# Kernel tuning notes

Measured on AMD Instinct MI355X. Metric: run time of the kernel, lower is better.

The kernel has to match this reference:

```python
import jax, jax.numpy as jnp
import numpy as np

N, D, K, H = 100000, 128, 16, 8
EPS = 1e-5


def setup_inputs() -> dict:
    key = jax.random.key(0)
    ks = jax.random.split(key, 8)
    s = 0.02
    return {
        "x": jax.random.normal(ks[0], (N, D), jnp.float32),
        "attention_samples": jax.random.randint(ks[1], (N, K), 0, N),
        "in_proj_w": jax.random.normal(ks[2], (3 * D, D), jnp.float32) * s,
        "in_proj_b": jnp.zeros((3 * D,), jnp.float32),
        "out_w": jax.random.normal(ks[3], (D, D), jnp.float32) * s,
        "out_b": jnp.zeros((D,), jnp.float32),
        "w1": jax.random.normal(ks[4], (4 * D, D), jnp.float32) * s,
        "b1": jnp.zeros((4 * D,), jnp.float32),
        "w2": jax.random.normal(ks[5], (D, 4 * D), jnp.float32) * s,
        "b2": jnp.zeros((D,), jnp.float32),
        "g1": jnp.ones((D,), jnp.float32),
        "be1": jnp.zeros((D,), jnp.float32),
        "g2": jnp.ones((D,), jnp.float32),
        "be2": jnp.zeros((D,), jnp.float32),
    }


def _layernorm(x, g, b):
    m = jnp.mean(x, axis=-1, keepdims=True)
    v = jnp.mean(jnp.square(x - m), axis=-1, keepdims=True)
    return (x - m) * jax.lax.rsqrt(v + EPS) * g + b


def reference(x, attention_samples, in_proj_w, in_proj_b, out_w, out_b,
              w1, b1, w2, b2, g1, be1, g2, be2):
    n, d = x.shape
    h = H
    hd = d // h
    wq, wk, wv = jnp.split(in_proj_w, 3, axis=0)
    bq, bk, bv = jnp.split(in_proj_b, 3, axis=0)
    # per-node query (q_len = 1)
    q = (x @ wq.T + bq).reshape(n, h, hd)            # [N,H,hd]
    samp = x[attention_samples]                       # [N,K,D] gathered neighbors
    k_ = (samp @ wk.T + bk).reshape(n, -1, h, hd)     # [N,K,H,hd]
    v_ = (samp @ wv.T + bv).reshape(n, -1, h, hd)
    scores = jnp.einsum('nhd,nkhd->nhk', q, k_) / jnp.sqrt(jnp.float32(hd))
    attn = jax.nn.softmax(scores, axis=-1)
    ctx = jnp.einsum('nhk,nkhd->nhd', attn, v_).reshape(n, d)
    attn_out = ctx @ out_w.T + out_b
    y = _layernorm(x + attn_out, g1, be1)
    ff = jax.nn.relu(y @ w1.T + b1) @ w2.T + b2
    return _layernorm(y + ff, g2, be2)
```

## Files before the change

kernel.cpp:

```cpp
#include <hip/hip_runtime.h>
#include <hip/hip_bf16.h>

typedef __attribute__((ext_vector_type(8))) short short8;
typedef __attribute__((ext_vector_type(4))) float f32x4;
typedef __attribute__((ext_vector_type(2))) float f32x2;

#define EPS 1e-5f

__device__ __forceinline__ unsigned short f2bf(float f) {
    union { float f; unsigned u; } v; v.f = f;
    unsigned u = v.u;
    u += 0x7FFFu + ((u >> 16) & 1u);
    return (unsigned short)(u >> 16);
}
__device__ __forceinline__ float bflo(unsigned u) {
    union { unsigned u; float f; } v; v.u = u << 16; return v.f;
}
__device__ __forceinline__ float bfhi(unsigned u) {
    union { unsigned u; float f; } v; v.u = u & 0xffff0000u; return v.f;
}
__device__ __forceinline__ float bf2f(ushort u) {
    union { unsigned u; float f; } v; v.u = ((unsigned)u) << 16; return v.f;
}
__device__ __forceinline__ unsigned char f2fp8(float v) {
    return (unsigned char)(__builtin_amdgcn_cvt_pk_fp8_f32(v, v, 0, false) & 0xff);
}
__device__ __forceinline__ int sig(int p) {
    return (((p >> 2) & 1) << 4) | (((p >> 3) & 3) << 2) | (p & 3);
}

__device__ __forceinline__ short8 load_frag_f32(const float* __restrict__ p) {
    f32x4 a = *(const f32x4*)p;
    f32x4 b = *(const f32x4*)(p + 4);
    short8 r;
    r[0] = (short)f2bf(a[0]); r[1] = (short)f2bf(a[1]);
    r[2] = (short)f2bf(a[2]); r[3] = (short)f2bf(a[3]);
    r[4] = (short)f2bf(b[0]); r[5] = (short)f2bf(b[1]);
    r[6] = (short)f2bf(b[2]); r[7] = (short)f2bf(b[3]);
    return r;
}

__device__ __forceinline__ float dot16_q_k8(const ushort* q, const unsigned char* kp) {
    uint4 kw = *(const uint4*)kp;
    const unsigned* qd = (const unsigned*)q;
    f32x2 a, b; float s = 0.f;
    a = __builtin_amdgcn_cvt_pk_f32_fp8(kw.x, false);
    b = __builtin_amdgcn_cvt_pk_f32_fp8(kw.x, true);
    s += a[0]*bflo(qd[0]) + a[1]*bfhi(qd[0]) + b[0]*bflo(qd[1]) + b[1]*bfhi(qd[1]);
    a = __builtin_amdgcn_cvt_pk_f32_fp8(kw.y, false);
    b = __builtin_amdgcn_cvt_pk_f32_fp8(kw.y, true);
    s += a[0]*bflo(qd[2]) + a[1]*bfhi(qd[2]) + b[0]*bflo(qd[3]) + b[1]*bfhi(qd[3]);
    a = __builtin_amdgcn_cvt_pk_f32_fp8(kw.z, false);
    b = __builtin_amdgcn_cvt_pk_f32_fp8(kw.z, true);
    s += a[0]*bflo(qd[4]) + a[1]*bfhi(qd[4]) + b[0]*bflo(qd[5]) + b[1]*bfhi(qd[5]);
    a = __builtin_amdgcn_cvt_pk_f32_fp8(kw.w, false);
    b = __builtin_amdgcn_cvt_pk_f32_fp8(kw.w, true);
    s += a[0]*bflo(qd[6]) + a[1]*bfhi(qd[6]) + b[0]*bflo(qd[7]) + b[1]*bfhi(qd[7]);
    return s;
}

__global__ __launch_bounds__(256) void k_prep(
        const float* __restrict__ ipw, const float* __restrict__ ow,
        const float* __restrict__ w1, const float* __restrict__ w2,
        ushort* __restrict__ wqb, ushort* __restrict__ wcat) {
    int i = blockIdx.x * 256 + threadIdx.x;
    if (i < 49152) wqb[i] = f2bf(ipw[i]);
    if (i < 147456) {
        float v;
        if (i < 8192) {
            int r = i >> 6, s = (i >> 3) & 7, e = i & 7;
            v = ow[r*128 + ((s ^ (r & 7)) << 3) + e];
        } else if (i < 16384) {
            int j = i - 8192;
            int r = j >> 6, s = (j >> 3) & 7, e = j & 7;
            v = ow[r*128 + 64 + ((s ^ (r & 7)) << 3) + e];
        } else {
            int j = i - 16384;
            int kb = j >> 13, o = j & 8191;
            if (o < 4096) {
                int r = (o >> 7) & 31, k16 = (o >> 3) & 15, e = o & 7;
                int cp = ((k16 ^ (r & 7)) << 3) + e;
                int cs = (cp & ~31) | sig(cp & 31);
                v = w1[(kb*32 + r)*128 + cs];
            } else {
                int oo = o - 4096;
                int ch = (oo >> 10) & 3, rw = (oo >> 3) & 127, e = oo & 7;
                v = w2[rw*512 + kb*32 + sig(ch*8 + e)];
            }
        }
        wcat[i] = f2bf(v);
    }
}

__global__ __launch_bounds__(256) void k_qkv(
        const float* __restrict__ x, const ushort* __restrict__ w,
        const float* __restrict__ bias, ushort* __restrict__ qt,
        unsigned char* __restrict__ kv8, ushort* __restrict__ xb, int N) {
    const int wave = threadIdx.x >> 6, lane = threadIdx.x & 63;
    const int l16 = lane & 15, l4 = lane >> 4;
    const int base = blockIdx.x * 64;

    short8 af[4][4];
    #pragma unroll
    for (int mt = 0; mt < 4; ++mt) {
        int row = base + mt*16 + l16;
        int rc = row < N ? row : N - 1;
        const float* p = x + (size_t)rc*128 + l4*8;
        #pragma unroll
        for (int kb = 0; kb < 4; ++kb) af[mt][kb] = load_frag_f32(p + kb*32);
    }
    #pragma unroll
    for (int mt = 0; mt < 4; ++mt) {
        int row = base + mt*16 + l16;
        if (row < N) {
            #pragma unroll
            for (int kb = 0; kb < 4; ++kb)
                *(short8*)(xb + (size_t)row*128 + kb*32 + l4*8) = af[mt][kb];
        }
    }
    #pragma unroll
    for (int i = 0; i < 6; ++i) {
        int col = (wave*6 + i)*16 + l16;
        const ushort* pw = w + (size_t)col*128 + l4*8;
        short8 bf[4];
        #pragma unroll
        for (int kb = 0; kb < 4; ++kb) bf[kb] = *(const short8*)(pw + kb*32);
        float bv = bias[col];
        #pragma unroll
        for (int mt = 0; mt < 4; ++mt) {
            f32x4 acc = {0.f, 0.f, 0.f, 0.f};
            #pragma unroll
            for (int kb = 0; kb < 4; ++kb)
                acc = __builtin_amdgcn_mfma_f32_16x16x32_bf16(af[mt][kb], bf[kb], acc, 0, 0, 0);
            #pragma unroll
            for (int r = 0; r < 4; ++r) {
                int row = base + mt*16 + l4*4 + r;
                if (row < N) {
                    float v = acc[r] + bv;
                    if (col < 128) qt[(size_t)row*128 + col] = f2bf(v);
                    else kv8[(size_t)row*256 + (col - 128)] = f2fp8(v);
                }
            }
        }
    }
}

__global__ __launch_bounds__(256) void k_attn(
        ushort* __restrict__ qt, const unsigned char* __restrict__ kv8,
        const int* __restrict__ samp, int N) {
    __shared__ float aw[4][8][17];
    __shared__ int   ai[4][16];
    const int wave = threadIdx.x >> 6, lane = threadIdx.x & 63;
    const int n = blockIdx.x * 4 + wave;
    if (n >= N) return;
    const int k  = lane & 15;
    const int hp = lane >> 4;
    const int h0 = hp, h1 = hp + 4;

    const int idx = samp[(size_t)n*16 + k];
    const ushort* qrow = qt + (size_t)n*128;
    const unsigned char* krow = kv8 + (size_t)idx*256;

    float s0 = dot16_q_k8(qrow + h0*16, krow + h0*16);
    float s1 = dot16_q_k8(qrow + h1*16, krow + h1*16);
    s0 *= 0.25f; s1 *= 0.25f;
    float m0 = s0, m1 = s1;
    #pragma unroll
    for (int off = 1; off < 16; off <<= 1) {
        m0 = fmaxf(m0, __shfl_xor(m0, off));
        m1 = fmaxf(m1, __shfl_xor(m1, off));
    }
    float e0 = __expf(s0 - m0), e1 = __expf(s1 - m1);
    float d0 = e0, d1 = e1;
    #pragma unroll
    for (int off = 1; off < 16; off <<= 1) {
        d0 += __shfl_xor(d0, off);
        d1 += __shfl_xor(d1, off);
    }
    aw[wave][h0][k] = e0 / d0;
    aw[wave][h1][k] = e1 / d1;
    if (hp == 0) ai[wave][k] = idx;

    const int c = lane & 15;
    const int g = lane >> 4;
    const int h = c >> 1;

    int rows[4];
    #pragma unroll
    for (int b = 0; b < 4; ++b) rows[b] = ai[wave][g + b*4];
    uint2 vv[4];
    #pragma unroll
    for (int b = 0; b < 4; ++b)
        vv[b] = *(const uint2*)(kv8 + (size_t)(unsigned)rows[b]*256 + 128 + c*8);
    float wk[4];
    #pragma unroll
    for (int b = 0; b < 4; ++b) wk[b] = aw[wave][h][g + b*4];

    float a8[8] = {0.f,0.f,0.f,0.f,0.f,0.f,0.f,0.f};
    #pragma unroll
    for (int b = 0; b < 4; ++b) {
        f32x2 p;
        p = __builtin_amdgcn_cvt_pk_f32_fp8(vv[b].x, false);
        a8[0] = fmaf(wk[b], p[0], a8[0]); a8[1] = fmaf(wk[b], p[1], a8[1]);
        p = __builtin_amdgcn_cvt_pk_f32_fp8(vv[b].x, true);
        a8[2] = fmaf(wk[b], p[0], a8[2]); a8[3] = fmaf(wk[b], p[1], a8[3]);
        p = __builtin_amdgcn_cvt_pk_f32_fp8(vv[b].y, false);
        a8[4] = fmaf(wk[b], p[0], a8[4]); a8[5] = fmaf(wk[b], p[1], a8[5]);
        p = __builtin_amdgcn_cvt_pk_f32_fp8(vv[b].y, true);
        a8[6] = fmaf(wk[b], p[0], a8[6]); a8[7] = fmaf(wk[b], p[1], a8[7]);
    }
    #pragma unroll
    for (int i = 0; i < 8; ++i) {
        a8[i] += __shfl_xor(a8[i], 16);
        a8[i] += __shfl_xor(a8[i], 32);
    }
    if (lane < 16) {
        uint4 pack;
        pack.x = (unsigned)f2bf(a8[0]) | ((unsigned)f2bf(a8[1]) << 16);
        pack.y = (unsigned)f2bf(a8[2]) | ((unsigned)f2bf(a8[3]) << 16);
        pack.z = (unsigned)f2bf(a8[4]) | ((unsigned)f2bf(a8[5]) << 16);
        pack.w = (unsigned)f2bf(a8[6]) | ((unsigned)f2bf(a8[7]) << 16);
        *(uint4*)(qt + (size_t)n*128 + c*8) = pack;
    }
}

__global__ __launch_bounds__(256) void k_tail(
        const ushort* __restrict__ ctx, const float* __restrict__ ob,
        const ushort* __restrict__ xb,
        const float* __restrict__ g1, const float* __restrict__ be1,
        const ushort* __restrict__ wcat, const float* __restrict__ b1,
        const float* __restrict__ b2,
        const float* __restrict__ g2, const float* __restrict__ be2,
        float* __restrict__ out, int N) {
    __shared__ __align__(16) char smem[32768];
    const int tid = threadIdx.x;
    const int lane = tid & 63;
    const int l16 = lane & 15, l4 = lane >> 4;
    const int base = blockIdx.x * 128 + (tid >> 6) * 32;
    int row[2], rc[2];
    row[0] = base + l16;       rc[0] = row[0] < N ? row[0] : N - 1;
    row[1] = base + 16 + l16;  rc[1] = row[1] < N ? row[1] : N - 1;

    uint4 nx0, nx1, nx2, nx3;
    const uint4* wc4 = (const uint4*)wcat;
#define STAGE_LOAD(cidx) { const uint4* s4 = wc4 + (cidx)*1024; \
    nx0 = s4[tid]; nx1 = s4[256 + tid]; nx2 = s4[512 + tid]; nx3 = s4[768 + tid]; }
#define STAGE_WRITE(cidx) { char* d = smem + (((cidx)&1) << 14); \
    *(uint4*)(d + tid*16) = nx0; *(uint4*)(d + (256 + tid)*16) = nx1; \
    *(uint4*)(d + (512 + tid)*16) = nx2; *(uint4*)(d + (768 + tid)*16) = nx3; }

    STAGE_LOAD(0); STAGE_WRITE(0); STAGE_LOAD(1);
    __syncthreads();

    f32x4 acc[2][8];
    #pragma unroll
    for (int mt = 0; mt < 2; ++mt)
        #pragma unroll
        for (int nt = 0; nt < 8; ++nt) acc[mt][nt] = (f32x4){0.f,0.f,0.f,0.f};

    #pragma unroll
    for (int ph = 0; ph < 2; ++ph) {
        STAGE_WRITE(ph + 1); STAGE_LOAD(ph + 2);
        short8 cfp[2][2];
        #pragma unroll
        for (int mt = 0; mt < 2; ++mt)
            #pragma unroll
            for (int j = 0; j < 2; ++j)
                cfp[mt][j] = *(const short8*)(ctx + (size_t)rc[mt]*128 + (ph*2 + j)*32 + l4*8);
        char* cur = smem + ((ph & 1) << 14);
        #pragma unroll
        for (int nt = 0; nt < 8; ++nt) {
            #pragma unroll
            for (int j = 0; j < 2; ++j) {
                int slot = (j*4 + l4) ^ (l16 & 7);
                short8 wf = *(const short8*)(cur + (nt*16 + l16)*128 + slot*16);
                acc[0][nt] = __builtin_amdgcn_mfma_f32_16x16x32_bf16(wf, cfp[0][j], acc[0][nt], 0, 0, 0);
                acc[1][nt] = __builtin_amdgcn_mfma_f32_16x16x32_bf16(wf, cfp[1][j], acc[1][nt], 0, 0, 0);
            }
        }
        __syncthreads();
    }

    float sum0 = 0.f, sq0 = 0.f, sum1 = 0.f, sq1 = 0.f;
    #pragma unroll
    for (int nt = 0; nt < 8; ++nt) {
        f32x4 obv = *(const f32x4*)(ob + nt*16 + l4*4);
        uint2 xr0 = *(const uint2*)(xb + (size_t)rc[0]*128 + nt*16 + l4*4);
        uint2 xr1 = *(const uint2*)(xb + (size_t)rc[1]*128 + nt*16 + l4*4);
        acc[0][nt][0] += obv[0] + bflo(xr0.x);
        acc[0][nt][1] += obv[1] + bfhi(xr0.x);
        acc[0][nt][2] += obv[2] + bflo(xr0.y);
        acc[0][nt][3] += obv[3] + bfhi(xr0.y);
        acc[1][nt][0] += obv[0] + bflo(xr1.x);
        acc[1][nt][1] += obv[1] + bfhi(xr1.x);
        acc[1][nt][2] += obv[2] + bflo(xr1.y);
        acc[1][nt][3] += obv[3] + bfhi(xr1.y);
        #pragma unroll
        for (int r = 0; r < 4; ++r) {
            sum0 += acc[0][nt][r]; sq0 += acc[0][nt][r]*acc[0][nt][r];
            sum1 += acc[1][nt][r]; sq1 += acc[1][nt][r]*acc[1][nt][r];
        }
    }
    sum0 += __shfl_xor(sum0, 16); sum0 += __shfl_xor(sum0, 32);
    sq0  += __shfl_xor(sq0, 16);  sq0  += __shfl_xor(sq0, 32);
    sum1 += __shfl_xor(sum1, 16); sum1 += __shfl_xor(sum1, 32);
    sq1  += __shfl_xor(sq1, 16);  sq1  += __shfl_xor(sq1, 32);
    float mean[2], rstd[2];
    mean[0] = sum0 * (1.f/128.f);
    rstd[0] = rsqrtf(sq0*(1.f/128.f) - mean[0]*mean[0] + EPS);
    mean[1] = sum1 * (1.f/128.f);
    rstd[1] = rsqrtf(sq1*(1.f/128.f) - mean[1]*mean[1] + EPS);

    short8 yfrag[2][4];
    #pragma unroll
    for (int nt = 0; nt < 8; ++nt) {
        f32x4 gv = *(const f32x4*)(g1 + nt*16 + l4*4);
        f32x4 bv = *(const f32x4*)(be1 + nt*16 + l4*4);
        #pragma unroll
        for (int mt = 0; mt < 2; ++mt)
            #pragma unroll
            for (int r = 0; r < 4; ++r) {
                float yn = (acc[mt][nt][r] - mean[mt]) * rstd[mt] * gv[r] + bv[r];
                yfrag[mt][nt >> 1][(nt & 1)*4 + r] = (short)f2bf(yn);
            }
    }

    f32x4 (&acc2)[2][8] = acc;
    #pragma unroll
    for (int mt = 0; mt < 2; ++mt)
        #pragma unroll
        for (int nt = 0; nt < 8; ++nt) acc2[mt][nt] = (f32x4){0.f,0.f,0.f,0.f};

    #pragma unroll 2
    for (int p = 2; p < 18; ++p) {
        if (p <= 16) { STAGE_WRITE(p + 1); }
        if (p <= 15) { STAGE_LOAD(p + 2); }
        const int kb = p - 2;
        char* cur = smem + ((p & 1) << 14);
        short8 wA[4], wB[4];
        #pragma unroll
        for (int c = 0; c < 4; ++c) {
            int slot = (c*4 + l4) ^ (l16 & 7);
            wA[c] = *(const short8*)(cur + l16*256 + slot*16);
            wB[c] = *(const short8*)(cur + 4096 + l16*256 + slot*16);
        }
        f32x4 hA[2] = {{0.f,0.f,0.f,0.f},{0.f,0.f,0.f,0.f}};
        f32x4 hB[2] = {{0.f,0.f,0.f,0.f},{0.f,0.f,0.f,0.f}};
        #pragma unroll
        for (int c = 0; c < 4; ++c)
            #pragma unroll
            for (int mt = 0; mt < 2; ++mt) {
                hA[mt] = __builtin_amdgcn_mfma_f32_16x16x32_bf16(wA[c], yfrag[mt][c], hA[mt], 0, 0, 0);
                hB[mt] = __builtin_amdgcn_mfma_f32_16x16x32_bf16(wB[c], yfrag[mt][c], hB[mt], 0, 0, 0);
            }
        f32x4 bA = *(const f32x4*)(b1 + kb*32 + l4*4);
        f32x4 bB = *(const f32x4*)(b1 + kb*32 + 16 + l4*4);
        short8 hf[2];
        #pragma unroll
        for (int mt = 0; mt < 2; ++mt)
            #pragma unroll
            for (int r = 0; r < 4; ++r) {
                float vA = hA[mt][r] + bA[r]; vA = vA > 0.f ? vA : 0.f;
                float vB = hB[mt][r] + bB[r]; vB = vB > 0.f ? vB : 0.f;
                hf[mt][r]     = (short)f2bf(vA);
                hf[mt][4 + r] = (short)f2bf(vB);
            }
        #pragma unroll
        for (int nt = 0; nt < 8; ++nt) {
            short8 w2f = *(const short8*)(cur + 8192 + l4*2048 + (nt*16 + l16)*16);
            acc2[0][nt] = __builtin_amdgcn_mfma_f32_16x16x32_bf16(w2f, hf[0], acc2[0][nt], 0, 0, 0);
            acc2[1][nt] = __builtin_amdgcn_mfma_f32_16x16x32_bf16(w2f, hf[1], acc2[1][nt], 0, 0, 0);
        }
        if (p < 17) __syncthreads();
    }

    #pragma unroll
    for (int mt = 0; mt < 2; ++mt) {
        float sum2 = 0.f, sq2 = 0.f;
        #pragma unroll
        for (int nt = 0; nt < 8; ++nt) {
            f32x4 b2v = *(const f32x4*)(b2 + nt*16 + l4*4);
            #pragma unroll
            for (int r = 0; r < 4; ++r) {
                float s = bf2f((ushort)yfrag[mt][nt >> 1][(nt & 1)*4 + r]) + acc2[mt][nt][r] + b2v[r];
                acc2[mt][nt][r] = s; sum2 += s; sq2 += s*s;
            }
        }
        sum2 += __shfl_xor(sum2, 16); sum2 += __shfl_xor(sum2, 32);
        sq2  += __shfl_xor(sq2, 16);  sq2  += __shfl_xor(sq2, 32);
        float mean2 = sum2 * (1.f/128.f);
        float rstd2 = rsqrtf(sq2*(1.f/128.f) - mean2*mean2 + EPS);
        if (row[mt] < N) {
            #pragma unroll
            for (int nt = 0; nt < 8; ++nt) {
                f32x4 gv = *(const f32x4*)(g2 + nt*16 + l4*4);
                f32x4 bv = *(const f32x4*)(be2 + nt*16 + l4*4);
                f32x4 o;
                #pragma unroll
                for (int r = 0; r < 4; ++r)
                    o[r] = (acc2[mt][nt][r] - mean2) * rstd2 * gv[r] + bv[r];
                *(f32x4*)(out + (size_t)row[mt]*128 + nt*16 + l4*4) = o;
            }
        }
    }
#undef STAGE_LOAD
#undef STAGE_WRITE
}

extern "C" void kernel_launch(void* const* d_in, const int* in_sizes, int n_in,
                              void* d_out, int out_size, void* d_ws, size_t ws_size,
                              hipStream_t stream) {
    (void)n_in; (void)out_size; (void)ws_size;
    const float* x   = (const float*)d_in[0];
    const int*   smp = (const int*)  d_in[1];
    const float* ipw = (const float*)d_in[2];
    const float* ipb = (const float*)d_in[3];
    const float* ow  = (const float*)d_in[4];
    const float* ob  = (const float*)d_in[5];
    const float* w1  = (const float*)d_in[6];
    const float* b1  = (const float*)d_in[7];
    const float* w2  = (const float*)d_in[8];
    const float* b2  = (const float*)d_in[9];
    const float* g1  = (const float*)d_in[10];
    const float* be1 = (const float*)d_in[11];
    const float* g2  = (const float*)d_in[12];
    const float* be2 = (const float*)d_in[13];
    const int N = in_sizes[0] / 128;

    ushort* qt   = (ushort*)d_ws;
    unsigned char* kv8 = (unsigned char*)(qt + (size_t)N*128);
    ushort* wqb  = (ushort*)(kv8 + (size_t)N*256);
    ushort* wcat = wqb + 384*128;
    ushort* xb   = wcat + 18*8192;
    float*  outp = (float*)d_out;

    k_prep <<<576,         256, 0, stream>>>(ipw, ow, w1, w2, wqb, wcat);
    k_qkv  <<<(N+63)/64,   256, 0, stream>>>(x, wqb, ipb, qt, kv8, xb, N);
    k_attn <<<(N+3)/4,     256, 0, stream>>>(qt, kv8, smp, N);
    k_tail <<<(N+127)/128, 256, 0, stream>>>(qt, ob, xb, g1, be1,
                                             wcat, b1, b2, g2, be2, outp, N);
}
```

Before: 236.5 us.

## Switch tail GEMMs to FP8 MFMA with resident weights and persistent blocks

Weights for out-proj, FFN1 and FFN2 are pre-scaled and stored as FP8, then loaded once into 144KB of LDS by a persistent 256-block, 512-thread tail kernel that loops over row tiles. The context vector is written as scaled FP8, and all tail matmuls use fp8 MFMA with rescaling afterwards. The qkv kernel also stages its outputs in shared memory so q and kv8 are written with coalesced vector stores. The aim is to halve weight and context traffic, remove per-stage weight streaming and barriers, and raise MFMA throughput, at the cost of FP8 accuracy loss in the activations and the FFN hidden layer.

```diff
diff --git a/kernel.cpp b/kernel.cpp
--- a/kernel.cpp
+++ b/kernel.cpp
@@ -24,6 +24,11 @@
 }
 __device__ __forceinline__ unsigned char f2fp8(float v) {
     return (unsigned char)(__builtin_amdgcn_cvt_pk_fp8_f32(v, v, 0, false) & 0xff);
+}
+__device__ __forceinline__ unsigned pk4fp8(float a, float b, float c, float d) {
+    unsigned u = __builtin_amdgcn_cvt_pk_fp8_f32(a, b, 0, false);
+    u = __builtin_amdgcn_cvt_pk_fp8_f32(c, d, u, true);
+    return u;
 }
 __device__ __forceinline__ int sig(int p) {
     return (((p >> 2) & 1) << 4) | (((p >> 3) & 3) << 2) | (p & 3);
@@ -62,33 +67,26 @@
 __global__ __launch_bounds__(256) void k_prep(
         const float* __restrict__ ipw, const float* __restrict__ ow,
         const float* __restrict__ w1, const float* __restrict__ w2,
-        ushort* __restrict__ wqb, ushort* __restrict__ wcat) {
+        ushort* __restrict__ wqb, unsigned char* __restrict__ wcat8) {
     int i = blockIdx.x * 256 + threadIdx.x;
     if (i < 49152) wqb[i] = f2bf(ipw[i]);
     if (i < 147456) {
         float v;
-        if (i < 8192) {
-            int r = i >> 6, s = (i >> 3) & 7, e = i & 7;
-            v = ow[r*128 + ((s ^ (r & 7)) << 3) + e];
-        } else if (i < 16384) {
-            int j = i - 8192;
-            int r = j >> 6, s = (j >> 3) & 7, e = j & 7;
-            v = ow[r*128 + 64 + ((s ^ (r & 7)) << 3) + e];
+        if (i < 16384) {
+            int r = i >> 7, s = (i >> 3) & 15, e = i & 7;
+            v = ow[r*128 + ((s ^ (r & 15)) << 3) + e];
+        } else if (i < 81920) {
+            int j = i - 16384;
+            int kb = j >> 12, r = (j >> 7) & 31, s = (j >> 3) & 15, e = j & 7;
+            int cp = ((s ^ (r & 15)) << 3) + e;
+            int cs = (cp & ~31) | sig(cp & 31);
+            v = w1[(kb*32 + r)*128 + cs];
         } else {
-            int j = i - 16384;
-            int kb = j >> 13, o = j & 8191;
-            if (o < 4096) {
-                int r = (o >> 7) & 31, k16 = (o >> 3) & 15, e = o & 7;
-                int cp = ((k16 ^ (r & 7)) << 3) + e;
-                int cs = (cp & ~31) | sig(cp & 31);
-                v = w1[(kb*32 + r)*128 + cs];
-            } else {
-                int oo = o - 4096;
-                int ch = (oo >> 10) & 3, rw = (oo >> 3) & 127, e = oo & 7;
-                v = w2[rw*512 + kb*32 + sig(ch*8 + e)];
-            }
-        }
-        wcat[i] = f2bf(v);
+            int j = i - 81920;
+            int kb = j >> 12, ch = (j >> 10) & 3, rw = (j >> 3) & 127, e = j & 7;
+            v = w2[rw*512 + kb*32 + sig(ch*8 + e)];
+        }
+        wcat8[i] = f2fp8(16.f * v);
     }
 }
 
@@ -96,6 +94,7 @@
         const float* __restrict__ x, const ushort* __restrict__ w,
         const float* __restrict__ bias, ushort* __restrict__ qt,
         unsigned char* __restrict__ kv8, ushort* __restrict__ xb, int N) {
+    __shared__ ushort sls[64 * 392];
     const int wave = threadIdx.x >> 6, lane = threadIdx.x & 63;
     const int l16 = lane & 15, l4 = lane >> 4;
     const int base = blockIdx.x * 64;
@@ -133,13 +132,31 @@
             for (int kb = 0; kb < 4; ++kb)
                 acc = __builtin_amdgcn_mfma_f32_16x16x32_bf16(af[mt][kb], bf[kb], acc, 0, 0, 0);
             #pragma unroll
-            for (int r = 0; r < 4; ++r) {
-                int row = base + mt*16 + l4*4 + r;
-                if (row < N) {
-                    float v = acc[r] + bv;
-                    if (col < 128) qt[(size_t)row*128 + col] = f2bf(v);
-                    else kv8[(size_t)row*256 + (col - 128)] = f2fp8(v);
-                }
+            for (int r = 0; r < 4; ++r)
+                sls[(mt*16 + l4*4 + r)*392 + col] = f2bf(acc[r] + bv);
+        }
+    }
+    __syncthreads();
+    {
+        const int row = threadIdx.x >> 2, q = threadIdx.x & 3;
+        const int grow = base + row;
+        if (grow < N) {
+            const ushort* sp = sls + row*392;
+            #pragma unroll
+            for (int j = 0; j < 4; ++j) {
+                uint4 v = *(const uint4*)(sp + q*32 + j*8);
+                *(uint4*)(qt + (size_t)grow*128 + q*32 + j*8) = v;
+            }
+            #pragma unroll
+            for (int j = 0; j < 4; ++j) {
+                unsigned wds[4];
+                #pragma unroll
+                for (int h = 0; h < 4; ++h) {
+                    const ushort* e = sp + 128 + q*64 + j*16 + h*4;
+                    wds[h] = pk4fp8(bf2f(e[0]), bf2f(e[1]), bf2f(e[2]), bf2f(e[3]));
+                }
+                *(uint4*)(kv8 + (size_t)grow*256 + q*64 + j*16) =
+                    make_uint4(wds[0], wds[1], wds[2], wds[3]);
             }
         }
     }
@@ -215,196 +232,201 @@
         a8[i] += __shfl_xor(a8[i], 32);
     }
     if (lane < 16) {
-        uint4 pack;
-        pack.x = (unsigned)f2bf(a8[0]) | ((unsigned)f2bf(a8[1]) << 16);
-        pack.y = (unsigned)f2bf(a8[2]) | ((unsigned)f2bf(a8[3]) << 16);
-        pack.z = (unsigned)f2bf(a8[4]) | ((unsigned)f2bf(a8[5]) << 16);
-        pack.w = (unsigned)f2bf(a8[6]) | ((unsigned)f2bf(a8[7]) << 16);
-        *(uint4*)(qt + (size_t)n*128 + c*8) = pack;
-    }
-}
-
-__global__ __launch_bounds__(256) void k_tail(
-        const ushort* __restrict__ ctx, const float* __restrict__ ob,
+        unsigned lo = pk4fp8(8.f*a8[0], 8.f*a8[1], 8.f*a8[2], 8.f*a8[3]);
+        unsigned hi = pk4fp8(8.f*a8[4], 8.f*a8[5], 8.f*a8[6], 8.f*a8[7]);
+        *(uint2*)((unsigned char*)qt + (size_t)n*256 + c*8) = make_uint2(lo, hi);
+    }
+}
+
+__global__ __launch_bounds__(512) void k_tail(
+        const unsigned char* __restrict__ ctx8, const float* __restrict__ ob,
         const ushort* __restrict__ xb,
         const float* __restrict__ g1, const float* __restrict__ be1,
-        const ushort* __restrict__ wcat, const float* __restrict__ b1,
+        const unsigned char* __restrict__ wcat8, const float* __restrict__ b1,
         const float* __restrict__ b2,
         const float* __restrict__ g2, const float* __restrict__ be2,
         float* __restrict__ out, int N) {
-    __shared__ __align__(16) char smem[32768];
+    __shared__ __align__(16) unsigned char smem[147456];
     const int tid = threadIdx.x;
-    const int lane = tid & 63;
+    const int wave = tid >> 6, lane = tid & 63;
     const int l16 = lane & 15, l4 = lane >> 4;
-    const int base = blockIdx.x * 128 + (tid >> 6) * 32;
-    int row[2], rc[2];
-    row[0] = base + l16;       rc[0] = row[0] < N ? row[0] : N - 1;
-    row[1] = base + 16 + l16;  rc[1] = row[1] < N ? row[1] : N - 1;
-
-    uint4 nx0, nx1, nx2, nx3;
-    const uint4* wc4 = (const uint4*)wcat;
-#define STAGE_LOAD(cidx) { const uint4* s4 = wc4 + (cidx)*1024; \
-    nx0 = s4[tid]; nx1 = s4[256 + tid]; nx2 = s4[512 + tid]; nx3 = s4[768 + tid]; }
-#define STAGE_WRITE(cidx) { char* d = smem + (((cidx)&1) << 14); \
-    *(uint4*)(d + tid*16) = nx0; *(uint4*)(d + (256 + tid)*16) = nx1; \
-    *(uint4*)(d + (512 + tid)*16) = nx2; *(uint4*)(d + (768 + tid)*16) = nx3; }
-
-    STAGE_LOAD(0); STAGE_WRITE(0); STAGE_LOAD(1);
+
+    {
+        const uint4* src = (const uint4*)wcat8;
+        #pragma unroll
+        for (int b = 0; b < 3; ++b) {
+            uint4 v[6];
+            #pragma unroll
+            for (int j = 0; j < 6; ++j) v[j] = src[(b*6 + j)*512 + tid];
+            #pragma unroll
+            for (int j = 0; j < 6; ++j)
+                *(uint4*)(smem + ((size_t)(b*6 + j)*512 + tid)*16) = v[j];
+        }
+    }
     __syncthreads();
 
-    f32x4 acc[2][8];
-    #pragma unroll
-    for (int mt = 0; mt < 2; ++mt)
-        #pragma unroll
-        for (int nt = 0; nt < 8; ++nt) acc[mt][nt] = (f32x4){0.f,0.f,0.f,0.f};
-
-    #pragma unroll
-    for (int ph = 0; ph < 2; ++ph) {
-        STAGE_WRITE(ph + 1); STAGE_LOAD(ph + 2);
-        short8 cfp[2][2];
+    const int ntiles = (N + 31) >> 5;
+    const int nwv = gridDim.x * 8;
+    for (int t = blockIdx.x * 8 + wave; t < ntiles; t += nwv) {
+        int row[2], rc[2];
+        row[0] = t*32 + l16;      rc[0] = row[0] < N ? row[0] : N - 1;
+        row[1] = t*32 + 16 + l16; rc[1] = row[1] < N ? row[1] : N - 1;
+
+        long cf[2][4];
         #pragma unroll
         for (int mt = 0; mt < 2; ++mt)
             #pragma unroll
-            for (int j = 0; j < 2; ++j)
-                cfp[mt][j] = *(const short8*)(ctx + (size_t)rc[mt]*128 + (ph*2 + j)*32 + l4*8);
-        char* cur = smem + ((ph & 1) << 14);
+            for (int c = 0; c < 4; ++c)
+                cf[mt][c] = *(const long*)(ctx8 + (size_t)rc[mt]*256 + c*32 + l4*8);
+        f32x4 acc[2][8];
+        #pragma unroll
+        for (int mt = 0; mt < 2; ++mt)
+            #pragma unroll
+            for (int nt = 0; nt < 8; ++nt) acc[mt][nt] = (f32x4){0.f,0.f,0.f,0.f};
         #pragma unroll
         for (int nt = 0; nt < 8; ++nt) {
             #pragma unroll
-            for (int j = 0; j < 2; ++j) {
-                int slot = (j*4 + l4) ^ (l16 & 7);
-                short8 wf = *(const short8*)(cur + (nt*16 + l16)*128 + slot*16);
-                acc[0][nt] = __builtin_amdgcn_mfma_f32_16x16x32_bf16(wf, cfp[0][j], acc[0][nt], 0, 0, 0);
-                acc[1][nt] = __builtin_amdgcn_mfma_f32_16x16x32_bf16(wf, cfp[1][j], acc[1][nt], 0, 0, 0);
-            }
-        }
-        __syncthreads();
-    }
-
-    float sum0 = 0.f, sq0 = 0.f, sum1 = 0.f, sq1 = 0.f;
-    #pragma unroll
-    for (int nt = 0; nt < 8; ++nt) {
-        f32x4 obv = *(const f32x4*)(ob + nt*16 + l4*4);
-        uint2 xr0 = *(const uint2*)(xb + (size_t)rc[0]*128 + nt*16 + l4*4);
-        uint2 xr1 = *(const uint2*)(xb + (size_t)rc[1]*128 + nt*16 + l4*4);
-        acc[0][nt][0] += obv[0] + bflo(xr0.x);
-        acc[0][nt][1] += obv[1] + bfhi(xr0.x);
-        acc[0][nt][2] += obv[2] + bflo(xr0.y);
-        acc[0][nt][3] += obv[3] + bfhi(xr0.y);
-        acc[1][nt][0] += obv[0] + bflo(xr1.x);
-        acc[1][nt][1] += obv[1] + bfhi(xr1.x);
-        acc[1][nt][2] += obv[2] + bflo(xr1.y);
-        acc[1][nt][3] += obv[3] + bfhi(xr1.y);
-        #pragma unroll
-        for (int r = 0; r < 4; ++r) {
-            sum0 += acc[0][nt][r]; sq0 += acc[0][nt][r]*acc[0][nt][r];
-            sum1 += acc[1][nt][r]; sq1 += acc[1][nt][r]*acc[1][nt][r];
-        }
-    }
-    sum0 += __shfl_xor(sum0, 16); sum0 += __shfl_xor(sum0, 32);
-    sq0  += __shfl_xor(sq0, 16);  sq0  += __shfl_xor(sq0, 32);
-    sum1 += __shfl_xor(sum1, 16); sum1 += __shfl_xor(sum1, 32);
-    sq1  += __shfl_xor(sq1, 16);  sq1  += __shfl_xor(sq1, 32);
-    float mean[2], rstd[2];
-    mean[0] = sum0 * (1.f/128.f);
-    rstd[0] = rsqrtf(sq0*(1.f/128.f) - mean[0]*mean[0] + EPS);
-    mean[1] = sum1 * (1.f/128.f);
-    rstd[1] = rsqrtf(sq1*(1.f/128.f) - mean[1]*mean[1] + EPS);
-
-    short8 yfrag[2][4];
-    #pragma unroll
-    for (int nt = 0; nt < 8; ++nt) {
-        f32x4 gv = *(const f32x4*)(g1 + nt*16 + l4*4);
-        f32x4 bv = *(const f32x4*)(be1 + nt*16 + l4*4);
+            for (int c = 0; c < 4; ++c) {
+                long wf = *(const long*)(smem + (nt*16 + l16)*128 + (((c*4 + l4) ^ l16) << 3));
+                acc[0][nt] = __builtin_amdgcn_mfma_f32_16x16x32_fp8_fp8(wf, cf[0][c], acc[0][nt], 0, 0, 0);
+                acc[1][nt] = __builtin_amdgcn_mfma_f32_16x16x32_fp8_fp8(wf, cf[1][c], acc[1][nt], 0, 0, 0);
+            }
+        }
+
+        float sum0 = 0.f, sq0 = 0.f, sum1 = 0.f, sq1 = 0.f;
+        #pragma unroll
+        for (int nt = 0; nt < 8; ++nt) {
+            f32x4 obv = *(const f32x4*)(ob + nt*16 + l4*4);
+            uint2 xr0 = *(const uint2*)(xb + (size_t)rc[0]*128 + nt*16 + l4*4);
+            uint2 xr1 = *(const uint2*)(xb + (size_t)rc[1]*128 + nt*16 + l4*4);
+            acc[0][nt][0] = acc[0][nt][0]*(1.f/128.f) + obv[0] + bflo(xr0.x);
+            acc[0][nt][1] = acc[0][nt][1]*(1.f/128.f) + obv[1] + bfhi(xr0.x);
+            acc[0][nt][2] = acc[0][nt][2]*(1.f/128.f) + obv[2] + bflo(xr0.y);
+            acc[0][nt][3] = acc[0][nt][3]*(1.f/128.f) + obv[3] + bfhi(xr0.y);
+            acc[1][nt][0] = acc[1][nt][0]*(1.f/128.f) + obv[0] + bflo(xr1.x);
+            acc[1][nt][1] = acc[1][nt][1]*(1.f/128.f) + obv[1] + bfhi(xr1.x);
+            acc[1][nt][2] = acc[1][nt][2]*(1.f/128.f) + obv[2] + bflo(xr1.y);
+            acc[1][nt][3] = acc[1][nt][3]*(1.f/128.f) + obv[3] + bfhi(xr1.y);
+            #pragma unroll
+            for (int r = 0; r < 4; ++r) {
+                sum0 += acc[0][nt][r]; sq0 += acc[0][nt][r]*acc[0][nt][r];
+                sum1 += acc[1][nt][r]; sq1 += acc[1][nt][r]*acc[1][nt][r];
+            }
+        }
+        sum0 += __shfl_xor(sum0, 16); sum0 += __shfl_xor(sum0, 32);
+        sq0  += __shfl_xor(sq0, 16);  sq0  += __shfl_xor(sq0, 32);
+        sum1 += __shfl_xor(sum1, 16); sum1 += __shfl_xor(sum1, 32);
+        sq1  += __shfl_xor(sq1, 16);  sq1  += __shfl_xor(sq1, 32);
+        float mean[2], rstd[2];
+        mean[0] = sum0 * (1.f/128.f);
+        rstd[0] = rsqrtf(sq0*(1.f/128.f) - mean[0]*mean[0] + EPS);
+        mean[1] = sum1 * (1.f/128.f);
+        rstd[1] = rsqrtf(sq1*(1.f/128.f) - mean[1]*mean[1] + EPS);
+
+        short8 yf16[2][4];
+        long   yf8[2][4];
+        #pragma unroll
+        for (int mt = 0; mt < 2; ++mt) {
+            #pragma unroll
+            for (int c = 0; c < 4; ++c) {
+                float yv[8];
+                #pragma unroll
+                for (int half = 0; half < 2; ++half) {
+                    int nt = 2*c + half;
+                    f32x4 gv = *(const f32x4*)(g1 + nt*16 + l4*4);
+                    f32x4 bv = *(const f32x4*)(be1 + nt*16 + l4*4);
+                    #pragma unroll
+                    for (int r = 0; r < 4; ++r) {
+                        float yn = (acc[mt][nt][r] - mean[mt]) * rstd[mt] * gv[r] + bv[r];
+                        yv[half*4 + r] = yn;
+                        yf16[mt][c][half*4 + r] = (short)f2bf(yn);
+                    }
+                }
+                unsigned lo = pk4fp8(yv[0], yv[1], yv[2], yv[3]);
+                unsigned hi = pk4fp8(yv[4], yv[5], yv[6], yv[7]);
+                yf8[mt][c] = (long)(((unsigned long long)hi << 32) | lo);
+            }
+        }
+
+        f32x4 acc2[2][8];
         #pragma unroll
         for (int mt = 0; mt < 2; ++mt)
             #pragma unroll
-            for (int r = 0; r < 4; ++r) {
-                float yn = (acc[mt][nt][r] - mean[mt]) * rstd[mt] * gv[r] + bv[r];
-                yfrag[mt][nt >> 1][(nt & 1)*4 + r] = (short)f2bf(yn);
-            }
-    }
-
-    f32x4 (&acc2)[2][8] = acc;
-    #pragma unroll
-    for (int mt = 0; mt < 2; ++mt)
-        #pragma unroll
-        for (int nt = 0; nt < 8; ++nt) acc2[mt][nt] = (f32x4){0.f,0.f,0.f,0.f};
-
-    #pragma unroll 2
-    for (int p = 2; p < 18; ++p) {
-        if (p <= 16) { STAGE_WRITE(p + 1); }
-        if (p <= 15) { STAGE_LOAD(p + 2); }
-        const int kb = p - 2;
-        char* cur = smem + ((p & 1) << 14);
-        short8 wA[4], wB[4];
-        #pragma unroll
-        for (int c = 0; c < 4; ++c) {
-            int slot = (c*4 + l4) ^ (l16 & 7);
-            wA[c] = *(const short8*)(cur + l16*256 + slot*16);
-            wB[c] = *(const short8*)(cur + 4096 + l16*256 + slot*16);
-        }
-        f32x4 hA[2] = {{0.f,0.f,0.f,0.f},{0.f,0.f,0.f,0.f}};
-        f32x4 hB[2] = {{0.f,0.f,0.f,0.f},{0.f,0.f,0.f,0.f}};
-        #pragma unroll
-        for (int c = 0; c < 4; ++c)
+            for (int nt = 0; nt < 8; ++nt) acc2[mt][nt] = (f32x4){0.f,0.f,0.f,0.f};
+        #pragma unroll 4
+        for (int kb = 0; kb < 16; ++kb) {
+            const unsigned char* w1b = smem + 16384 + kb*4096;
+            long wA[4], wB[4];
+            #pragma unroll
+            for (int c = 0; c < 4; ++c) {
+                int so = ((c*4 + l4) ^ l16) << 3;
+                wA[c] = *(const long*)(w1b + l16*128 + so);
+                wB[c] = *(const long*)(w1b + (16 + l16)*128 + so);
+            }
+            f32x4 hA[2] = {{0.f,0.f,0.f,0.f},{0.f,0.f,0.f,0.f}};
+            f32x4 hB[2] = {{0.f,0.f,0.f,0.f},{0.f,0.f,0.f,0.f}};
+            #pragma unroll
+            for (int c = 0; c < 4; ++c)
+                #pragma unroll
+                for (int mt = 0; mt < 2; ++mt) {
+                    hA[mt] = __builtin_amdgcn_mfma_f32_16x16x32_fp8_fp8(wA[c], yf8[mt][c], hA[mt], 0, 0, 0);
+                    hB[mt] = __builtin_amdgcn_mfma_f32_16x16x32_fp8_fp8(wB[c], yf8[mt][c], hB[mt], 0, 0, 0);
+                }
+            f32x4 bA = *(const f32x4*)(b1 + kb*32 + l4*4);
+            f32x4 bB = *(const f32x4*)(b1 + kb*32 + 16 + l4*4);
+            long hf8[2];
             #pragma unroll
             for (int mt = 0; mt < 2; ++mt) {
-                hA[mt] = __builtin_amdgcn_mfma_f32_16x16x32_bf16(wA[c], yfrag[mt][c], hA[mt], 0, 0, 0);
-                hB[mt] = __builtin_amdgcn_mfma_f32_16x16x32_bf16(wB[c], yfrag[mt][c], hB[mt], 0, 0, 0);
-            }
-        f32x4 bA = *(const f32x4*)(b1 + kb*32 + l4*4);
-        f32x4 bB = *(const f32x4*)(b1 + kb*32 + 16 + l4*4);
-        short8 hf[2];
-        #pragma unroll
-        for (int mt = 0; mt < 2; ++mt)
-            #pragma unroll
-            for (int r = 0; r < 4; ++r) {
-                float vA = hA[mt][r] + bA[r]; vA = vA > 0.f ? vA : 0.f;
-                float vB = hB[mt][r] + bB[r]; vB = vB > 0.f ? vB : 0.f;
-                hf[mt][r]     = (short)f2bf(vA);
-                hf[mt][4 + r] = (short)f2bf(vB);
-            }
-        #pragma unroll
-        for (int nt = 0; nt < 8; ++nt) {
-            short8 w2f = *(const short8*)(cur + 8192 + l4*2048 + (nt*16 + l16)*16);
-            acc2[0][nt] = __builtin_amdgcn_mfma_f32_16x16x32_bf16(w2f, hf[0], acc2[0][nt], 0, 0, 0);
-            acc2[1][nt] = __builtin_amdgcn_mfma_f32_16x16x32_bf16(w2f, hf[1], acc2[1][nt], 0, 0, 0);
-        }
-        if (p < 17) __syncthreads();
-    }
-
-    #pragma unroll
-    for (int mt = 0; mt < 2; ++mt) {
-        float sum2 = 0.f, sq2 = 0.f;
-        #pragma unroll
-        for (int nt = 0; nt < 8; ++nt) {
-            f32x4 b2v = *(const f32x4*)(b2 + nt*16 + l4*4);
-            #pragma unroll
-            for (int r = 0; r < 4; ++r) {
-                float s = bf2f((ushort)yfrag[mt][nt >> 1][(nt & 1)*4 + r]) + acc2[mt][nt][r] + b2v[r];
-                acc2[mt][nt][r] = s; sum2 += s; sq2 += s*s;
-            }
-        }
-        sum2 += __shfl_xor(sum2, 16); sum2 += __shfl_xor(sum2, 32);
-        sq2  += __shfl_xor(sq2, 16);  sq2  += __shfl_xor(sq2, 32);
-        float mean2 = sum2 * (1.f/128.f);
-        float rstd2 = rsqrtf(sq2*(1.f/128.f) - mean2*mean2 + EPS);
-        if (row[mt] < N) {
+                float vA[4], vB[4];
+                #pragma unroll
+                for (int r = 0; r < 4; ++r) {
+                    vA[r] = fmaxf(hA[mt][r]*0.0625f + bA[r], 0.f);
+                    vB[r] = fmaxf(hB[mt][r]*0.0625f + bB[r], 0.f);
+                }
+                unsigned lo = pk4fp8(vA[0], vA[1], vA[2], vA[3]);
+                unsigned hi = pk4fp8(vB[0], vB[1], vB[2], vB[3]);
+                hf8[mt] = (long)(((unsigned long long)hi << 32) | lo);
+            }
+            const unsigned char* w2b = smem + 81920 + kb*4096 + l4*1024;
             #pragma unroll
             for (int nt = 0; nt < 8; ++nt) {
-                f32x4 gv = *(const f32x4*)(g2 + nt*16 + l4*4);
-                f32x4 bv = *(const f32x4*)(be2 + nt*16 + l4*4);
-                f32x4 o;
-                #pragma unroll
-                for (int r = 0; r < 4; ++r)
-                    o[r] = (acc2[mt][nt][r] - mean2) * rstd2 * gv[r] + bv[r];
-                *(f32x4*)(out + (size_t)row[mt]*128 + nt*16 + l4*4) = o;
-            }
-        }
-    }
-#undef STAGE_LOAD
-#undef STAGE_WRITE
+                long w2f = *(const long*)(w2b + (nt*16 + l16)*8);
+                acc2[0][nt] = __builtin_amdgcn_mfma_f32_16x16x32_fp8_fp8(w2f, hf8[0], acc2[0][nt], 0, 0, 0);
+                acc2[1][nt] = __builtin_amdgcn_mfma_f32_16x16x32_fp8_fp8(w2f, hf8[1], acc2[1][nt], 0, 0, 0);
+            }
+        }
+
+        #pragma unroll
+        for (int mt = 0; mt < 2; ++mt) {
+            float sum2 = 0.f, sq2 = 0.f;
+            #pragma unroll
+            for (int nt = 0; nt < 8; ++nt) {
+                f32x4 b2v = *(const f32x4*)(b2 + nt*16 + l4*4);
+                #pragma unroll
+                for (int r = 0; r < 4; ++r) {
+                    float s = bf2f((ushort)yf16[mt][nt >> 1][(nt & 1)*4 + r])
+                              + acc2[mt][nt][r]*0.0625f + b2v[r];
+                    acc2[mt][nt][r] = s; sum2 += s; sq2 += s*s;
+                }
+            }
+            sum2 += __shfl_xor(sum2, 16); sum2 += __shfl_xor(sum2, 32);
+            sq2  += __shfl_xor(sq2, 16);  sq2  += __shfl_xor(sq2, 32);
+            float mean2 = sum2 * (1.f/128.f);
+            float rstd2 = rsqrtf(sq2*(1.f/128.f) - mean2*mean2 + EPS);
+            if (row[mt] < N) {
+                #pragma unroll
+                for (int nt = 0; nt < 8; ++nt) {
+                    f32x4 gv = *(const f32x4*)(g2 + nt*16 + l4*4);
+                    f32x4 bv = *(const f32x4*)(be2 + nt*16 + l4*4);
+                    f32x4 o;
+                    #pragma unroll
+                    for (int r = 0; r < 4; ++r)
+                        o[r] = (acc2[mt][nt][r] - mean2) * rstd2 * gv[r] + bv[r];
+                    *(f32x4*)(out + (size_t)row[mt]*128 + nt*16 + l4*4) = o;
+                }
+            }
+        }
+    }
 }
 
 extern "C" void kernel_launch(void* const* d_in, const int* in_sizes, int n_in,
@@ -430,13 +452,13 @@
     ushort* qt   = (ushort*)d_ws;
     unsigned char* kv8 = (unsigned char*)(qt + (size_t)N*128);
     ushort* wqb  = (ushort*)(kv8 + (size_t)N*256);
-    ushort* wcat = wqb + 384*128;
-    ushort* xb   = wcat + 18*8192;
+    unsigned char* wcat8 = (unsigned char*)(wqb + 49152);
+    ushort* xb   = (ushort*)(wcat8 + 147456);
     float*  outp = (float*)d_out;
 
-    k_prep <<<576,         256, 0, stream>>>(ipw, ow, w1, w2, wqb, wcat);
-    k_qkv  <<<(N+63)/64,   256, 0, stream>>>(x, wqb, ipb, qt, kv8, xb, N);
-    k_attn <<<(N+3)/4,     256, 0, stream>>>(qt, kv8, smp, N);
-    k_tail <<<(N+127)/128, 256, 0, stream>>>(qt, ob, xb, g1, be1,
-                                             wcat, b1, b2, g2, be2, outp, N);
-}
+    k_prep <<<576,       256, 0, stream>>>(ipw, ow, w1, w2, wqb, wcat8);
+    k_qkv  <<<(N+63)/64, 256, 0, stream>>>(x, wqb, ipb, qt, kv8, xb, N);
+    k_attn <<<(N+3)/4,   256, 0, stream>>>(qt, kv8, smp, N);
+    k_tail <<<256,       512, 0, stream>>>((const unsigned char*)qt, ob, xb, g1, be1,
+                                           wcat8, b1, b2, g2, be2, outp, N);
+}
```

Result: faster. 212.9 us (-10.0%).
